# Performance work log

Measured on AMD Instinct MI355X. Metric: run time of the kernel, lower is better.

Reference implementation:

```python
import jax, jax.numpy as jnp
import numpy as np

TOP_K = 2

def setup_inputs() -> dict:
    key = jax.random.key(0)
    k0, k1, k2, k3 = jax.random.split(key, 4)
    B, S, D, F, E = 4, 4096, 1024, 2048, 8
    x = jax.random.normal(k0, (B, S, D), dtype=jnp.float32)
    w_router = jax.random.normal(k1, (E, D), dtype=jnp.float32) * 0.02
    w1 = jax.random.normal(k2, (E, F, D), dtype=jnp.float32) * 0.02
    w2 = jax.random.normal(k3, (E, D, F), dtype=jnp.float32) * 0.02
    return {"x": x, "w_router": w_router, "w1": w1, "w2": w2}

def reference(x, w_router, w1, w2):
    # x: [B,S,D]; w_router: [E,D]; w1: [E,F,D]; w2: [E,D,F]
    B, S, D = x.shape
    E = w_router.shape[0]
    xf = x.reshape(-1, D)                      # [T,D], T = B*S
    T = xf.shape[0]
    logits = xf @ w_router.T                   # [T,E]
    probs = jax.nn.softmax(logits, axis=-1)    # [T,E]
    top_v, top_i = jax.lax.top_k(probs, TOP_K) # [T,K]
    top_v = top_v / jnp.sum(top_v, axis=-1, keepdims=True)
    # dense combine weights: w[t,e] = renormalized prob if e in top-k else 0
    comb = jnp.zeros_like(probs).at[jnp.arange(T)[:, None], top_i].add(top_v)  # [T,E]
    # dense per-expert compute, masked/weighted combine (same math as gather-MLP-scatter;
    # dropout is identity in eval). GELU is exact (erf), matching torch F.gelu default.
    out = jnp.zeros_like(xf)
    for e in range(E):  # small fixed expert loop
        h = jax.nn.gelu(xf @ w1[e].T, approximate=False)   # [T,F]
        out = out + comb[:, e:e + 1] * (h @ w2[e].T)       # [T,D]
    expert_usage = jnp.mean(probs, axis=0)                  # [E]
    aux_loss = E * jnp.sum(expert_usage ** 2)
    return out.reshape(B, S, D), aux_loss
```

## Files before the change

kernel.cpp:

```cpp
#include <hip/hip_runtime.h>
#include <hip/hip_bf16.h>
#include <math.h>

typedef __attribute__((ext_vector_type(8))) short s16x8;
typedef __attribute__((ext_vector_type(4))) float f32x4;

#define T_TOK 16384
#define D_DIM 1024
#define F_DIM 2048
#define E_NUM 8
#define RCAP 34816

__device__ __forceinline__ unsigned short f2b(float f) {
  unsigned u = __float_as_uint(f);
  u += 0x7fff + ((u >> 16) & 1);
  return (unsigned short)(u >> 16);
}
__device__ __forceinline__ float b2f(unsigned short h) {
  return __uint_as_float(((unsigned)h) << 16);
}
__device__ __forceinline__ unsigned pk2(float a, float b) {
  __hip_bfloat162 h = __float22bfloat162_rn(make_float2(a, b));
  return *reinterpret_cast<unsigned*>(&h);
}
__device__ __forceinline__ float gelu_f(float v) {
  float x = v * 0.70710678118f;
  float ax = fabsf(x);
  float t = __builtin_amdgcn_rcpf(1.f + 0.3275911f * ax);
  float y = t * (0.254829592f +
           t * (-0.284496736f +
           t * (1.421413741f +
           t * (-1.453152027f +
           t * 1.061405429f))));
  float e = __expf(-x * x);
  float er = 1.f - y * e;
  er = (x < 0.f) ? -er : er;
  return 0.5f * v * (1.f + er);
}

__global__ void castw_k(const float* __restrict__ w1, const float* __restrict__ w2,
                        unsigned short* __restrict__ w1b, unsigned short* __restrict__ w2b) {
  size_t i = ((size_t)blockIdx.x * 256 + threadIdx.x) * 4;
  float4 a = *(const float4*)(w1 + i);
  float4 b = *(const float4*)(w2 + i);
  uint2 ua, ub;
  ua.x = pk2(a.x, a.y); ua.y = pk2(a.z, a.w);
  ub.x = pk2(b.x, b.y); ub.y = pk2(b.z, b.w);
  *(uint2*)(w1b + i) = ua;
  *(uint2*)(w2b + i) = ub;
}

__global__ void router_k(const float* __restrict__ x, const float* __restrict__ wr,
                         int* __restrict__ topi, float* __restrict__ topw,
                         float* __restrict__ probs8, unsigned short* __restrict__ xb) {
  int tid = threadIdx.x, wid = tid >> 6, lane = tid & 63;
  int t = blockIdx.x * 4 + wid;
  const float* xr = x + (size_t)t * D_DIM;
  float4 xv[4];
#pragma unroll
  for (int i = 0; i < 4; ++i) xv[i] = *(const float4*)(xr + i * 256 + lane * 4);
#pragma unroll
  for (int i = 0; i < 4; ++i) {
    uint2 u; u.x = pk2(xv[i].x, xv[i].y); u.y = pk2(xv[i].z, xv[i].w);
    *(uint2*)(xb + (size_t)t * D_DIM + i * 256 + lane * 4) = u;
  }
  float logit[E_NUM];
#pragma unroll
  for (int e = 0; e < E_NUM; ++e) {
    const float* wrow = wr + e * D_DIM;
    float p = 0.f;
#pragma unroll
    for (int i = 0; i < 4; ++i) {
      float4 wv = *(const float4*)(wrow + i * 256 + lane * 4);
      p += xv[i].x * wv.x + xv[i].y * wv.y + xv[i].z * wv.z + xv[i].w * wv.w;
    }
    for (int s = 32; s; s >>= 1) p += __shfl_xor(p, s);
    logit[e] = p;
  }
  if (lane == 0) {
    float m = logit[0];
    for (int e = 1; e < E_NUM; ++e) m = fmaxf(m, logit[e]);
    float pr[E_NUM];
    float sum = 0.f;
    for (int e = 0; e < E_NUM; ++e) { pr[e] = expf(logit[e] - m); sum += pr[e]; }
    float inv = 1.f / sum;
    for (int e = 0; e < E_NUM; ++e) { pr[e] *= inv; probs8[t * 8 + e] = pr[e]; }
    int i0 = 0;
    for (int e = 1; e < E_NUM; ++e) if (pr[e] > pr[i0]) i0 = e;
    int i1 = (i0 == 0) ? 1 : 0;
    for (int e = 0; e < E_NUM; ++e) if (e != i0 && pr[e] > pr[i1]) i1 = e;
    float wsum = pr[i0] + pr[i1];
    topi[2 * t] = i0;  topi[2 * t + 1] = i1;
    topw[2 * t] = pr[i0] / wsum;  topw[2 * t + 1] = pr[i1] / wsum;
  }
}

__global__ void hist_k(const int* __restrict__ topi, const float* __restrict__ probs8,
                       int* __restrict__ cnt, float* __restrict__ usage) {
  __shared__ int sc[E_NUM];
  __shared__ float su[E_NUM];
  int tid = threadIdx.x;
  if (tid < E_NUM) { sc[tid] = 0; su[tid] = 0.f; }
  __syncthreads();
  for (int i = blockIdx.x * 256 + tid; i < 2 * T_TOK; i += 256 * 64)
    atomicAdd(&sc[topi[i]], 1);
  for (int i = blockIdx.x * 256 + tid; i < 8 * T_TOK; i += 256 * 64)
    atomicAdd(&su[i & 7], probs8[i]);
  __syncthreads();
  if (tid < E_NUM) { atomicAdd(&cnt[tid], sc[tid]); atomicAdd(&usage[tid], su[tid]); }
}

__global__ void scan_k(const int* __restrict__ cnt, int* __restrict__ offs,
                       const float* __restrict__ usage, float* __restrict__ aux) {
  if (threadIdx.x == 0 && blockIdx.x == 0) {
    int o = 0;
    for (int e = 0; e < E_NUM; ++e) { offs[e] = o; o += (cnt[e] + 255) & ~255; }
    offs[E_NUM] = o;
    float s = 0.f;
    for (int e = 0; e < E_NUM; ++e) { float m = usage[e] * (1.f / T_TOK); s += m * m; }
    *aux = (float)E_NUM * s;
  }
}

__global__ void assign_k(const int* __restrict__ topi, const int* __restrict__ offs,
                         int* __restrict__ cur, int* __restrict__ rowpair) {
  int p = blockIdx.x * 256 + threadIdx.x;
  int lane = threadIdx.x & 63;
  int e = topi[p];
  int r = 0;
#pragma unroll
  for (int ee = 0; ee < E_NUM; ++ee) {
    unsigned long long mask = __ballot(e == ee);
    if (e == ee) {
      int leader = __ffsll((unsigned long long)mask) - 1;
      int rank = __popcll(mask & ((1ull << lane) - 1ull));
      int b = 0;
      if (lane == leader) b = atomicAdd(&cur[ee], (int)__popcll(mask));
      b = __shfl(b, leader);
      r = offs[ee] + b + rank;
    }
  }
  rowpair[r] = p;
}


#define RGEMM_BODY(NT, EPILOGUE)                                               \
  f32x4 acc[4][4] = {};                                                        \
  s16x8 rA[4], rB[4];                                                          \
  _Pragma("unroll") for (int i = 0; i < 4; ++i) {                              \
    rA[i] = *(const s16x8*)(pA[i]);                                            \
    rB[i] = *(const s16x8*)(pB[i]);                                            \
  }                                                                            \
  _Pragma("unroll 2")                                                          \
  for (int t = 0; t < NT; ++t) {                                               \
    if (t) __syncthreads();                                                    \
    _Pragma("unroll") for (int i = 0; i < 4; ++i) {                            \
      *(s16x8*)&As[wo[i]] = rA[i];                                             \
      *(s16x8*)&Bs[wo[i]] = rB[i];                                             \
    }                                                                          \
    __syncthreads();                                                           \
    if (t < NT - 1) {                                                          \
      int k0 = (t + 1) * 64;                                                   \
      _Pragma("unroll") for (int i = 0; i < 4; ++i) {                          \
        rA[i] = *(const s16x8*)(pA[i] + k0);                                   \
        rB[i] = *(const s16x8*)(pB[i] + k0);                                   \
      }                                                                        \
    }                                                                          \
    int ar = wm * 64 + rl, br = wn * 64 + rl;                                  \
    _Pragma("unroll") for (int kk = 0; kk < 2; ++kk) {                         \
      int cs = (((kk * 4 + g4) ^ (rl & 7)) << 3);                              \
      s16x8 a[4], b[4];                                                        \
      _Pragma("unroll") for (int m = 0; m < 4; ++m)                            \
        a[m] = *(const s16x8*)&As[(ar + m * 16) * 64 + cs];                    \
      _Pragma("unroll") for (int n = 0; n < 4; ++n)                            \
        b[n] = *(const s16x8*)&Bs[(br + n * 16) * 64 + cs];                    \
      __builtin_amdgcn_s_setprio(1);                                           \
      _Pragma("unroll") for (int m = 0; m < 4; ++m)                            \
        _Pragma("unroll") for (int n = 0; n < 4; ++n)                          \
          acc[m][n] = __builtin_amdgcn_mfma_f32_16x16x32_bf16(                 \
              a[m], b[n], acc[m][n], 0, 0, 0);                                 \
      __builtin_amdgcn_s_setprio(0);                                           \
    }                                                                          \
  }                                                                            \
  EPILOGUE

__global__ __launch_bounds__(256, 3) void gemm1v_k(
    const unsigned short* __restrict__ xb, const unsigned short* __restrict__ w1b,
    const int* __restrict__ offs, const int* __restrict__ rowpair,
    const unsigned short* __restrict__ zrow,
    unsigned short* __restrict__ hseg, int segbase, int segrows) {
  int bid0 = blockIdx.x;
  int bid = ((bid0 & 7) << 11) | (bid0 >> 3);
  int e = bid >> 11, rem = bid & 2047, mt = rem >> 4, nt = rem & 15;
  int rend = offs[e + 1];
  int rowbase = offs[e] + mt * 128;
  if (rowbase >= rend || rowbase < segbase || rowbase >= segbase + segrows) return;

  __shared__ short As[128 * 64];
  __shared__ short Bs[128 * 64];
  int tid = threadIdx.x, wid = tid >> 6, lane = tid & 63;
  int wm = wid >> 1, wn = wid & 1, rl = lane & 15, g4 = lane >> 4;
  int j7 = tid & 7, rr = tid >> 3;
  int wg = ((j7 ^ (rr & 7)) << 3);
  int wo[4];
#pragma unroll
  for (int i = 0; i < 4; ++i) wo[i] = (rr + i * 32) * 64 + wg;

  const unsigned short* pA[4];
  const unsigned short* pB[4];
#pragma unroll
  for (int i = 0; i < 4; ++i) {
    int p = rowpair[rowbase + rr + i * 32];
    pA[i] = (p >= 0 ? xb + (size_t)(p >> 1) * D_DIM : zrow) + j7 * 8;
    pB[i] = w1b + ((size_t)e * F_DIM + nt * 128 + rr + i * 32) * D_DIM + j7 * 8;
  }

  RGEMM_BODY(16, {
    size_t rloc = (size_t)(rowbase - segbase);
    int c0 = nt * 128 + wn * 64 + rl;
    int lr0 = wm * 64 + (g4 << 2);
    _Pragma("unroll") for (int m = 0; m < 4; ++m)
      _Pragma("unroll") for (int j = 0; j < 4; ++j) {
        size_t rrow = (rloc + lr0 + m * 16 + j) * F_DIM;
        _Pragma("unroll") for (int n = 0; n < 4; ++n)
          hseg[rrow + c0 + n * 16] = f2b(gelu_f(acc[m][n][j]));
      }
  })
}

__global__ __launch_bounds__(256, 3) void gemm2s_k(
    const unsigned short* __restrict__ hseg, const unsigned short* __restrict__ w2b,
    const int* __restrict__ offs, const int* __restrict__ rowpair,
    unsigned short* __restrict__ obuf, int segbase, int segrows) {
  int bid0 = blockIdx.x;
  int bid = ((bid0 & 7) << 10) | (bid0 >> 3);
  int e = bid >> 10, rem = bid & 1023, mt = rem >> 3, nt = rem & 7;
  int rend = offs[e + 1];
  int rowbase = offs[e] + mt * 128;
  if (rowbase >= rend || rowbase < segbase || rowbase >= segbase + segrows) return;

  __shared__ short As[128 * 64];
  __shared__ short Bs[128 * 64];
  int tid = threadIdx.x, wid = tid >> 6, lane = tid & 63;
  int wm = wid >> 1, wn = wid & 1, rl = lane & 15, g4 = lane >> 4;
  int j7 = tid & 7, rr = tid >> 3;
  int wg = ((j7 ^ (rr & 7)) << 3);
  int wo[4];
#pragma unroll
  for (int i = 0; i < 4; ++i) wo[i] = (rr + i * 32) * 64 + wg;

  size_t rloc = (size_t)(rowbase - segbase);
  const unsigned short* pA[4];
  const unsigned short* pB[4];
#pragma unroll
  for (int i = 0; i < 4; ++i) {
    pA[i] = hseg + (rloc + rr + i * 32) * F_DIM + j7 * 8;
    pB[i] = w2b + ((size_t)e * D_DIM + nt * 128 + rr + i * 32) * F_DIM + j7 * 8;
  }

  RGEMM_BODY(32, {
    int c0 = nt * 128 + wn * 64 + rl;
    int lr0 = wm * 64 + (g4 << 2);
    _Pragma("unroll") for (int m = 0; m < 4; ++m)
      _Pragma("unroll") for (int j = 0; j < 4; ++j) {
        int lr = lr0 + m * 16 + j;
        int p = rowpair[rowbase + lr];
        if (p >= 0) {
          unsigned short* op = obuf + (size_t)p * D_DIM + c0;
          _Pragma("unroll") for (int n = 0; n < 4; ++n)
            op[n * 16] = f2b(acc[m][n][j]);
        }
      }
  })
}

__global__ __launch_bounds__(256, 3) void gemm2v_k(
    const unsigned short* __restrict__ hseg, const unsigned short* __restrict__ w2b,
    const int* __restrict__ offs, const int* __restrict__ rowpair,
    const float* __restrict__ topw, float* __restrict__ out,
    int segbase, int segrows) {
  int bid0 = blockIdx.x;
  int bid = ((bid0 & 7) << 10) | (bid0 >> 3);
  int e = bid >> 10, rem = bid & 1023, mt = rem >> 3, nt = rem & 7;
  int rend = offs[e + 1];
  int rowbase = offs[e] + mt * 128;
  if (rowbase >= rend || rowbase < segbase || rowbase >= segbase + segrows) return;

  __shared__ short As[128 * 64];
  __shared__ short Bs[128 * 64];
  int tid = threadIdx.x, wid = tid >> 6, lane = tid & 63;
  int wm = wid >> 1, wn = wid & 1, rl = lane & 15, g4 = lane >> 4;
  int j7 = tid & 7, rr = tid >> 3;
  int wg = ((j7 ^ (rr & 7)) << 3);
  int wo[4];
#pragma unroll
  for (int i = 0; i < 4; ++i) wo[i] = (rr + i * 32) * 64 + wg;

  size_t rloc = (size_t)(rowbase - segbase);
  const unsigned short* pA[4];
  const unsigned short* pB[4];
#pragma unroll
  for (int i = 0; i < 4; ++i) {
    pA[i] = hseg + (rloc + rr + i * 32) * F_DIM + j7 * 8;
    pB[i] = w2b + ((size_t)e * D_DIM + nt * 128 + rr + i * 32) * F_DIM + j7 * 8;
  }

  RGEMM_BODY(32, {
    int c0 = nt * 128 + wn * 64 + rl;
    int lr0 = wm * 64 + (g4 << 2);
    _Pragma("unroll") for (int m = 0; m < 4; ++m)
      _Pragma("unroll") for (int j = 0; j < 4; ++j) {
        int lr = lr0 + m * 16 + j;
        int p = rowpair[rowbase + lr];
        if (p >= 0) {
          float wgt = topw[p];
          float* op = out + (size_t)(p >> 1) * D_DIM + c0;
          _Pragma("unroll") for (int n = 0; n < 4; ++n)
            unsafeAtomicAdd(op + n * 16, wgt * acc[m][n][j]);
        }
      }
  })
}

__global__ void combine_k(const unsigned short* __restrict__ obuf,
                          const float* __restrict__ topw, float* __restrict__ out) {
  int u = blockIdx.x * 256 + threadIdx.x;
  int t = u >> 7;
  int d0 = (u & 127) * 8;
  float w0 = topw[2 * t], w1 = topw[2 * t + 1];
  s16x8 a = *(const s16x8*)(obuf + (size_t)(2 * t) * D_DIM + d0);
  s16x8 b = *(const s16x8*)(obuf + (size_t)(2 * t + 1) * D_DIM + d0);
  float r[8];
#pragma unroll
  for (int j = 0; j < 8; ++j)
    r[j] = w0 * b2f((unsigned short)a[j]) + w1 * b2f((unsigned short)b[j]);
  float4 lo = {r[0], r[1], r[2], r[3]};
  float4 hi = {r[4], r[5], r[6], r[7]};
  float* o = out + (size_t)t * D_DIM + d0;
  *(float4*)o = lo;
  *(float4*)(o + 4) = hi;
}

extern "C" void kernel_launch(void* const* d_in, const int* in_sizes, int n_in,
                              void* d_out, int out_size, void* d_ws, size_t ws_size,
                              hipStream_t stream) {
  const float* x  = (const float*)d_in[0];
  const float* wr = (const float*)d_in[1];
  const float* w1 = (const float*)d_in[2];
  const float* w2 = (const float*)d_in[3];
  float* out = (float*)d_out;

  char* ws = (char*)d_ws;
  int* cnt   = (int*)ws;
  int* cur   = cnt + 8;
  int* offs  = cnt + 16;
  float* usage = (float*)(cnt + 25);
  unsigned short* zrow = (unsigned short*)(ws + 4096);
  size_t off = 8192;
  int*   topi = (int*)(ws + off);     off += (size_t)2 * T_TOK * 4;
  float* topw = (float*)(ws + off);   off += (size_t)2 * T_TOK * 4;
  int*   rowpair = (int*)(ws + off);  off += (size_t)RCAP * 4;
  float* probs8 = (float*)(ws + off); off += (size_t)T_TOK * 8 * 4;
  off = (off + 255) & ~(size_t)255;

  unsigned short* xb = (unsigned short*)(ws + off);
  off += (size_t)T_TOK * D_DIM * 2;
  unsigned short* w1b = (unsigned short*)(ws + off);
  off += (size_t)E_NUM * F_DIM * D_DIM * 2;
  unsigned short* w2b = (unsigned short*)(ws + off);
  off += (size_t)E_NUM * F_DIM * D_DIM * 2;
  if (ws_size < off + (size_t)4096 * F_DIM * 2) return;
  size_t avail = ws_size - off;
  size_t segcap = (avail / ((size_t)F_DIM * 2)) & ~(size_t)255;
  int segrows = segcap > (size_t)RCAP ? RCAP : (int)segcap;
  unsigned short* hseg = (unsigned short*)(ws + off);
  int nseg = (RCAP + segrows - 1) / segrows;

  bool storepath = (nseg == 1);
  unsigned short* obuf = xb;

  hipMemsetAsync(ws, 0, 8192, stream);
  hipMemsetAsync(rowpair, 0xFF, (size_t)RCAP * 4, stream);
  if (!storepath) hipMemsetAsync(d_out, 0, (size_t)out_size * 4, stream);
  castw_k<<<16384, 256, 0, stream>>>(w1, w2, w1b, w2b);
  router_k<<<T_TOK / 4, 256, 0, stream>>>(x, wr, topi, topw, probs8, xb);
  hist_k<<<64, 256, 0, stream>>>(topi, probs8, cnt, usage);
  scan_k<<<1, 64, 0, stream>>>(cnt, offs, usage, out + (size_t)T_TOK * D_DIM);
  assign_k<<<2 * T_TOK / 256, 256, 0, stream>>>(topi, offs, cur, rowpair);

  for (int s = 0; s < nseg; ++s) {
    int segbase = s * segrows;
    gemm1v_k<<<16384, 256, 0, stream>>>(xb, w1b, offs, rowpair, zrow, hseg, segbase, segrows);
    if (storepath)
      gemm2s_k<<<8192, 256, 0, stream>>>(hseg, w2b, offs, rowpair, obuf, segbase, segrows);
    else
      gemm2v_k<<<8192, 256, 0, stream>>>(hseg, w2b, offs, rowpair, topw, out, segbase, segrows);
  }
  if (storepath)
    combine_k<<<T_TOK * D_DIM / 8 / 256, 256, 0, stream>>>(obuf, topw, out);
}
```

Before: 501.6 us.

## Enlarge grouped GEMM tiles to 256x128 with K-step 32 per stage

Reworks the grouped expert GEMMs to use 256-row by 128-column block tiles with a 32-wide K slice per stage instead of 128x128 with 64-wide K. Each wave now computes a 128x64 sub-tile with 8x4 MFMA accumulators, reusing each B fragment across eight A fragments to raise arithmetic intensity. The swizzle, LDS layout and grid sizes are adjusted to match. This doubles accumulator registers and drops the occupancy hint of three blocks per SM. Halving the K depth per stage also doubles the number of barriers, and the larger row tiles waste more padding at expert boundaries.

```diff
diff --git a/kernel.cpp b/kernel.cpp
--- a/kernel.cpp
+++ b/kernel.cpp
@@ -144,179 +144,184 @@
 }
 
 
-#define RGEMM_BODY(NT, EPILOGUE)                                               \
-  f32x4 acc[4][4] = {};                                                        \
-  s16x8 rA[4], rB[4];                                                          \
-  _Pragma("unroll") for (int i = 0; i < 4; ++i) {                              \
-    rA[i] = *(const s16x8*)(pA[i]);                                            \
-    rB[i] = *(const s16x8*)(pB[i]);                                            \
-  }                                                                            \
+#define RGW_BODY(NT, EPILOGUE)                                                 \
+  f32x4 acc[8][4] = {};                                                        \
+  s16x8 rA[4], rB[2];                                                          \
+  _Pragma("unroll") for (int i = 0; i < 4; ++i) rA[i] = *(const s16x8*)(pA[i]);\
+  _Pragma("unroll") for (int i = 0; i < 2; ++i) rB[i] = *(const s16x8*)(pB[i]);\
   _Pragma("unroll 2")                                                          \
   for (int t = 0; t < NT; ++t) {                                               \
     if (t) __syncthreads();                                                    \
-    _Pragma("unroll") for (int i = 0; i < 4; ++i) {                            \
-      *(s16x8*)&As[wo[i]] = rA[i];                                             \
-      *(s16x8*)&Bs[wo[i]] = rB[i];                                             \
-    }                                                                          \
+    _Pragma("unroll") for (int i = 0; i < 4; ++i) *(s16x8*)&As[woA[i]] = rA[i];\
+    _Pragma("unroll") for (int i = 0; i < 2; ++i) *(s16x8*)&Bs[woB[i]] = rB[i];\
     __syncthreads();                                                           \
     if (t < NT - 1) {                                                          \
-      int k0 = (t + 1) * 64;                                                   \
-      _Pragma("unroll") for (int i = 0; i < 4; ++i) {                          \
+      int k0 = (t + 1) * 32;                                                   \
+      _Pragma("unroll") for (int i = 0; i < 4; ++i)                            \
         rA[i] = *(const s16x8*)(pA[i] + k0);                                   \
+      _Pragma("unroll") for (int i = 0; i < 2; ++i)                            \
         rB[i] = *(const s16x8*)(pB[i] + k0);                                   \
-      }                                                                        \
     }                                                                          \
-    int ar = wm * 64 + rl, br = wn * 64 + rl;                                  \
-    _Pragma("unroll") for (int kk = 0; kk < 2; ++kk) {                         \
-      int cs = (((kk * 4 + g4) ^ (rl & 7)) << 3);                              \
-      s16x8 a[4], b[4];                                                        \
-      _Pragma("unroll") for (int m = 0; m < 4; ++m)                            \
-        a[m] = *(const s16x8*)&As[(ar + m * 16) * 64 + cs];                    \
+    s16x8 b[4];                                                                \
+    _Pragma("unroll") for (int n = 0; n < 4; ++n)                              \
+      b[n] = *(const s16x8*)&Bs[(wn * 64 + n * 16 + rl) * 32 + cs];            \
+    _Pragma("unroll") for (int mm = 0; mm < 8; ++mm) {                         \
+      s16x8 a = *(const s16x8*)&As[(wm * 128 + mm * 16 + rl) * 32 + cs];       \
+      __builtin_amdgcn_s_setprio(1);                                           \
       _Pragma("unroll") for (int n = 0; n < 4; ++n)                            \
-        b[n] = *(const s16x8*)&Bs[(br + n * 16) * 64 + cs];                    \
-      __builtin_amdgcn_s_setprio(1);                                           \
-      _Pragma("unroll") for (int m = 0; m < 4; ++m)                            \
-        _Pragma("unroll") for (int n = 0; n < 4; ++n)                          \
-          acc[m][n] = __builtin_amdgcn_mfma_f32_16x16x32_bf16(                 \
-              a[m], b[n], acc[m][n], 0, 0, 0);                                 \
+        acc[mm][n] = __builtin_amdgcn_mfma_f32_16x16x32_bf16(                  \
+            a, b[n], acc[mm][n], 0, 0, 0);                                     \
       __builtin_amdgcn_s_setprio(0);                                           \
     }                                                                          \
   }                                                                            \
   EPILOGUE
 
-__global__ __launch_bounds__(256, 3) void gemm1v_k(
+__global__ __launch_bounds__(256) void gemm1x_k(
     const unsigned short* __restrict__ xb, const unsigned short* __restrict__ w1b,
     const int* __restrict__ offs, const int* __restrict__ rowpair,
     const unsigned short* __restrict__ zrow,
     unsigned short* __restrict__ hseg, int segbase, int segrows) {
   int bid0 = blockIdx.x;
-  int bid = ((bid0 & 7) << 11) | (bid0 >> 3);
-  int e = bid >> 11, rem = bid & 2047, mt = rem >> 4, nt = rem & 15;
+  int bid = ((bid0 & 7) << 10) | (bid0 >> 3);
+  int e = bid >> 10, rem = bid & 1023, mt = rem >> 4, nt = rem & 15;
   int rend = offs[e + 1];
-  int rowbase = offs[e] + mt * 128;
+  int rowbase = offs[e] + mt * 256;
   if (rowbase >= rend || rowbase < segbase || rowbase >= segbase + segrows) return;
 
-  __shared__ short As[128 * 64];
-  __shared__ short Bs[128 * 64];
+  __shared__ short As[256 * 32];
+  __shared__ short Bs[128 * 32];
   int tid = threadIdx.x, wid = tid >> 6, lane = tid & 63;
   int wm = wid >> 1, wn = wid & 1, rl = lane & 15, g4 = lane >> 4;
-  int j7 = tid & 7, rr = tid >> 3;
-  int wg = ((j7 ^ (rr & 7)) << 3);
-  int wo[4];
-#pragma unroll
-  for (int i = 0; i < 4; ++i) wo[i] = (rr + i * 32) * 64 + wg;
+  int gw = tid & 3, rr2 = tid >> 2;
+  int wkey = (gw ^ (rr2 & 3)) << 3;
+  int cs = ((g4 ^ (rl & 3)) << 3);
+  int woA[4], woB[2];
+#pragma unroll
+  for (int i = 0; i < 4; ++i) woA[i] = (rr2 + i * 64) * 32 + wkey;
+#pragma unroll
+  for (int i = 0; i < 2; ++i) woB[i] = (rr2 + i * 64) * 32 + wkey;
 
   const unsigned short* pA[4];
-  const unsigned short* pB[4];
+  const unsigned short* pB[2];
 #pragma unroll
   for (int i = 0; i < 4; ++i) {
-    int p = rowpair[rowbase + rr + i * 32];
-    pA[i] = (p >= 0 ? xb + (size_t)(p >> 1) * D_DIM : zrow) + j7 * 8;
-    pB[i] = w1b + ((size_t)e * F_DIM + nt * 128 + rr + i * 32) * D_DIM + j7 * 8;
-  }
-
-  RGEMM_BODY(16, {
+    int p = rowpair[rowbase + rr2 + i * 64];
+    pA[i] = (p >= 0 ? xb + (size_t)(p >> 1) * D_DIM : zrow) + gw * 8;
+  }
+#pragma unroll
+  for (int i = 0; i < 2; ++i)
+    pB[i] = w1b + ((size_t)e * F_DIM + nt * 128 + rr2 + i * 64) * D_DIM + gw * 8;
+
+  RGW_BODY(32, {
     size_t rloc = (size_t)(rowbase - segbase);
     int c0 = nt * 128 + wn * 64 + rl;
-    int lr0 = wm * 64 + (g4 << 2);
-    _Pragma("unroll") for (int m = 0; m < 4; ++m)
+    int lr0 = wm * 128 + (g4 << 2);
+    _Pragma("unroll") for (int mm = 0; mm < 8; ++mm)
       _Pragma("unroll") for (int j = 0; j < 4; ++j) {
-        size_t rrow = (rloc + lr0 + m * 16 + j) * F_DIM;
+        size_t rrow = (rloc + lr0 + mm * 16 + j) * F_DIM;
         _Pragma("unroll") for (int n = 0; n < 4; ++n)
-          hseg[rrow + c0 + n * 16] = f2b(gelu_f(acc[m][n][j]));
+          hseg[rrow + c0 + n * 16] = f2b(gelu_f(acc[mm][n][j]));
       }
   })
 }
 
-__global__ __launch_bounds__(256, 3) void gemm2s_k(
+__global__ __launch_bounds__(256) void gemm2x_k(
     const unsigned short* __restrict__ hseg, const unsigned short* __restrict__ w2b,
     const int* __restrict__ offs, const int* __restrict__ rowpair,
     unsigned short* __restrict__ obuf, int segbase, int segrows) {
   int bid0 = blockIdx.x;
-  int bid = ((bid0 & 7) << 10) | (bid0 >> 3);
-  int e = bid >> 10, rem = bid & 1023, mt = rem >> 3, nt = rem & 7;
+  int bid = ((bid0 & 7) << 9) | (bid0 >> 3);
+  int e = bid >> 9, rem = bid & 511, mt = rem >> 3, nt = rem & 7;
   int rend = offs[e + 1];
-  int rowbase = offs[e] + mt * 128;
+  int rowbase = offs[e] + mt * 256;
   if (rowbase >= rend || rowbase < segbase || rowbase >= segbase + segrows) return;
 
-  __shared__ short As[128 * 64];
-  __shared__ short Bs[128 * 64];
+  __shared__ short As[256 * 32];
+  __shared__ short Bs[128 * 32];
   int tid = threadIdx.x, wid = tid >> 6, lane = tid & 63;
   int wm = wid >> 1, wn = wid & 1, rl = lane & 15, g4 = lane >> 4;
-  int j7 = tid & 7, rr = tid >> 3;
-  int wg = ((j7 ^ (rr & 7)) << 3);
-  int wo[4];
-#pragma unroll
-  for (int i = 0; i < 4; ++i) wo[i] = (rr + i * 32) * 64 + wg;
+  int gw = tid & 3, rr2 = tid >> 2;
+  int wkey = (gw ^ (rr2 & 3)) << 3;
+  int cs = ((g4 ^ (rl & 3)) << 3);
+  int woA[4], woB[2];
+#pragma unroll
+  for (int i = 0; i < 4; ++i) woA[i] = (rr2 + i * 64) * 32 + wkey;
+#pragma unroll
+  for (int i = 0; i < 2; ++i) woB[i] = (rr2 + i * 64) * 32 + wkey;
 
   size_t rloc = (size_t)(rowbase - segbase);
   const unsigned short* pA[4];
-  const unsigned short* pB[4];
-#pragma unroll
-  for (int i = 0; i < 4; ++i) {
-    pA[i] = hseg + (rloc + rr + i * 32) * F_DIM + j7 * 8;
-    pB[i] = w2b + ((size_t)e * D_DIM + nt * 128 + rr + i * 32) * F_DIM + j7 * 8;
-  }
-
-  RGEMM_BODY(32, {
+  const unsigned short* pB[2];
+#pragma unroll
+  for (int i = 0; i < 4; ++i)
+    pA[i] = hseg + (rloc + rr2 + i * 64) * F_DIM + gw * 8;
+#pragma unroll
+  for (int i = 0; i < 2; ++i)
+    pB[i] = w2b + ((size_t)e * D_DIM + nt * 128 + rr2 + i * 64) * F_DIM + gw * 8;
+
+  RGW_BODY(64, {
     int c0 = nt * 128 + wn * 64 + rl;
-    int lr0 = wm * 64 + (g4 << 2);
-    _Pragma("unroll") for (int m = 0; m < 4; ++m)
+    int lr0 = wm * 128 + (g4 << 2);
+    _Pragma("unroll") for (int mm = 0; mm < 8; ++mm)
       _Pragma("unroll") for (int j = 0; j < 4; ++j) {
-        int lr = lr0 + m * 16 + j;
+        int lr = lr0 + mm * 16 + j;
         int p = rowpair[rowbase + lr];
         if (p >= 0) {
           unsigned short* op = obuf + (size_t)p * D_DIM + c0;
           _Pragma("unroll") for (int n = 0; n < 4; ++n)
-            op[n * 16] = f2b(acc[m][n][j]);
+            op[n * 16] = f2b(acc[mm][n][j]);
         }
       }
   })
 }
 
-__global__ __launch_bounds__(256, 3) void gemm2v_k(
+__global__ __launch_bounds__(256) void gemm2y_k(
     const unsigned short* __restrict__ hseg, const unsigned short* __restrict__ w2b,
     const int* __restrict__ offs, const int* __restrict__ rowpair,
     const float* __restrict__ topw, float* __restrict__ out,
     int segbase, int segrows) {
   int bid0 = blockIdx.x;
-  int bid = ((bid0 & 7) << 10) | (bid0 >> 3);
-  int e = bid >> 10, rem = bid & 1023, mt = rem >> 3, nt = rem & 7;
+  int bid = ((bid0 & 7) << 9) | (bid0 >> 3);
+  int e = bid >> 9, rem = bid & 511, mt = rem >> 3, nt = rem & 7;
   int rend = offs[e + 1];
-  int rowbase = offs[e] + mt * 128;
+  int rowbase = offs[e] + mt * 256;
   if (rowbase >= rend || rowbase < segbase || rowbase >= segbase + segrows) return;
 
-  __shared__ short As[128 * 64];
-  __shared__ short Bs[128 * 64];
+  __shared__ short As[256 * 32];
+  __shared__ short Bs[128 * 32];
   int tid = threadIdx.x, wid = tid >> 6, lane = tid & 63;
   int wm = wid >> 1, wn = wid & 1, rl = lane & 15, g4 = lane >> 4;
-  int j7 = tid & 7, rr = tid >> 3;
-  int wg = ((j7 ^ (rr & 7)) << 3);
-  int wo[4];
-#pragma unroll
-  for (int i = 0; i < 4; ++i) wo[i] = (rr + i * 32) * 64 + wg;
+  int gw = tid & 3, rr2 = tid >> 2;
+  int wkey = (gw ^ (rr2 & 3)) << 3;
+  int cs = ((g4 ^ (rl & 3)) << 3);
+  int woA[4], woB[2];
+#pragma unroll
+  for (int i = 0; i < 4; ++i) woA[i] = (rr2 + i * 64) * 32 + wkey;
+#pragma unroll
+  for (int i = 0; i < 2; ++i) woB[i] = (rr2 + i * 64) * 32 + wkey;
 
   size_t rloc = (size_t)(rowbase - segbase);
   const unsigned short* pA[4];
-  const unsigned short* pB[4];
-#pragma unroll
-  for (int i = 0; i < 4; ++i) {
-    pA[i] = hseg + (rloc + rr + i * 32) * F_DIM + j7 * 8;
-    pB[i] = w2b + ((size_t)e * D_DIM + nt * 128 + rr + i * 32) * F_DIM + j7 * 8;
-  }
-
-  RGEMM_BODY(32, {
+  const unsigned short* pB[2];
+#pragma unroll
+  for (int i = 0; i < 4; ++i)
+    pA[i] = hseg + (rloc + rr2 + i * 64) * F_DIM + gw * 8;
+#pragma unroll
+  for (int i = 0; i < 2; ++i)
+    pB[i] = w2b + ((size_t)e * D_DIM + nt * 128 + rr2 + i * 64) * F_DIM + gw * 8;
+
+  RGW_BODY(64, {
     int c0 = nt * 128 + wn * 64 + rl;
-    int lr0 = wm * 64 + (g4 << 2);
-    _Pragma("unroll") for (int m = 0; m < 4; ++m)
+    int lr0 = wm * 128 + (g4 << 2);
+    _Pragma("unroll") for (int mm = 0; mm < 8; ++mm)
       _Pragma("unroll") for (int j = 0; j < 4; ++j) {
-        int lr = lr0 + m * 16 + j;
+        int lr = lr0 + mm * 16 + j;
         int p = rowpair[rowbase + lr];
         if (p >= 0) {
           float wgt = topw[p];
           float* op = out + (size_t)(p >> 1) * D_DIM + c0;
           _Pragma("unroll") for (int n = 0; n < 4; ++n)
-            unsafeAtomicAdd(op + n * 16, wgt * acc[m][n][j]);
+            unsafeAtomicAdd(op + n * 16, wgt * acc[mm][n][j]);
         }
       }
   })
@@ -390,11 +395,11 @@
 
   for (int s = 0; s < nseg; ++s) {
     int segbase = s * segrows;
-    gemm1v_k<<<16384, 256, 0, stream>>>(xb, w1b, offs, rowpair, zrow, hseg, segbase, segrows);
+    gemm1x_k<<<8192, 256, 0, stream>>>(xb, w1b, offs, rowpair, zrow, hseg, segbase, segrows);
     if (storepath)
-      gemm2s_k<<<8192, 256, 0, stream>>>(hseg, w2b, offs, rowpair, obuf, segbase, segrows);
+      gemm2x_k<<<4096, 256, 0, stream>>>(hseg, w2b, offs, rowpair, obuf, segbase, segrows);
     else
-      gemm2v_k<<<8192, 256, 0, stream>>>(hseg, w2b, offs, rowpair, topw, out, segbase, segrows);
+      gemm2y_k<<<4096, 256, 0, stream>>>(hseg, w2b, offs, rowpair, topw, out, segbase, segrows);
   }
   if (storepath)
     combine_k<<<T_TOK * D_DIM / 8 / 256, 256, 0, stream>>>(obuf, topw, out);
```

Result: slower. 688.4 us (+37.3%).
